# Optimization experiments

Measured on AMD Instinct MI355X. Metric: run time of the kernel, lower is better.

The kernel has to match this reference:

```python
import jax, jax.numpy as jnp
import numpy as np

B, S, D = 64, 512, 768
H, DK, DV = 3, 64, 64
TAG, NBEST = 33, 8
START, STOP = TAG - 2, TAG - 1
NEG = -1e30
LN_EPS = 1e-3


def setup_inputs():
    ks = jax.random.split(jax.random.key(0), 10)
    sc = 0.02
    lengths = jax.random.randint(ks[1], (B,), S // 2, S + 1)
    trans = jax.random.normal(ks[8], (TAG, TAG), jnp.float32) * 0.1
    # NCRF++ constraints: nothing transitions INTO START; nothing OUT of STOP
    trans = trans.at[:, START].set(-10000.0).at[STOP, :].set(-10000.0)
    return {
        "inputs": jax.random.normal(ks[0], (B, S, D), jnp.float32),
        "labels_mask": (jnp.arange(S)[None, :] < lengths[:, None]).astype(jnp.int32),
        "w_qs": jax.random.normal(ks[2], (H, D, DK), jnp.float32) * sc,
        "w_ks": jax.random.normal(ks[3], (H, D, DK), jnp.float32) * sc,
        "w_vs": jax.random.normal(ks[4], (H, D, DV), jnp.float32) * sc,
        "proj_w": jax.random.normal(ks[5], (H * DV, D), jnp.float32) * sc,
        "proj_b": jnp.zeros((D,), jnp.float32),
        "ln_g": jnp.ones((D,), jnp.float32),
        "ln_b": jnp.zeros((D,), jnp.float32),
        "lin1_w": jax.random.normal(ks[6], (D, D // 2), jnp.float32) * sc,
        "lin1_b": jnp.zeros((D // 2,), jnp.float32),
        "lin2_w": jax.random.normal(ks[7], (D // 2, TAG), jnp.float32) * sc,
        "lin2_b": jnp.zeros((TAG,), jnp.float32),
        "transitions": trans,
    }


def _layer_norm(x, g, b):
    mu = jnp.mean(x, -1, keepdims=True)
    sig = jnp.std(x, -1, keepdims=True, ddof=1)  # repo LayerNorm uses unbiased std, eps=1e-3
    return (x - mu) / (sig + LN_EPS) * g + b


def _forward_model(x, w_qs, w_ks, w_vs, proj_w, proj_b, ln_g, ln_b, lin1_w, lin1_b, lin2_w, lin2_b):
    # multi-head attention (mask=None on this path; dropout off: module calls self.eval())
    q = jnp.einsum("bsd,hdk->bhsk", x, w_qs)
    k = jnp.einsum("bsd,hdk->bhsk", x, w_ks)
    v = jnp.einsum("bsd,hdv->bhsv", x, w_vs)
    attn = jax.nn.softmax(jnp.einsum("bhqk,bhtk->bhqt", q, k) / np.float32(np.sqrt(DK)), axis=-1)
    o = jnp.einsum("bhqt,bhtv->bqhv", attn, v).reshape(B, S, H * DV)
    o = _layer_norm(o @ proj_w + proj_b + x, ln_g, ln_b)  # proj + residual + LN
    h = jnp.tanh(o @ lin1_w + lin1_b)                      # Linears hidden (tanh)
    return h @ lin2_w + lin2_b                             # (B, S, TAG)


def _viterbi_dp(logits, mask, transitions):
    # scores[t,b,from,to] = logits[t,b,to] + transitions[from,to]
    scores = logits.transpose(1, 0, 2)[:, :, None, :] + transitions[None, None]  # (S,B,T,T)
    # step-0 partition: only nbest slot 0 is live (NEG elsewhere reproduces torch's idx==1 special case)
    partition0 = jnp.full((B, TAG, NBEST), NEG, logits.dtype).at[:, :, 0].set(scores[0, :, START, :])
    mask_t = mask.astype(jnp.int32).T  # (S, B)

    def step(partition, xs):
        sc_t, m_t = xs  # (B,T,T), (B,)
        cand = (sc_t[:, :, None, :] + partition[:, :, :, None]).reshape(B, TAG * NBEST, TAG)
        vals, idx = jax.lax.top_k(cand.transpose(0, 2, 1), NBEST)  # (B, to, NBEST) over from*nbest
        bp = jnp.where(m_t[:, None, None] > 0, idx, 0)
        return vals, (vals, bp)

    _, (parts, bps) = jax.lax.scan(step, partition0, (scores[1:], mask_t[1:]))
    ph = jnp.concatenate([partition0[None], parts], 0).transpose(1, 0, 2, 3)  # (B,S,T,N)
    last_pos = mask_t.sum(0) - 1  # (B,)
    last_partition = jnp.take_along_axis(ph, last_pos[:, None, None, None], axis=1)[:, 0]  # (B,T,N)
    last_values = (last_partition[:, :, :, None] + transitions[None, :, None, :]).reshape(B, TAG * NBEST, TAG)
    end_vals, end_bp = jax.lax.top_k(last_values.transpose(0, 2, 1), NBEST)  # (B, to, NBEST)
    path_score = jax.nn.softmax(end_vals[:, STOP, :], axis=1)  # (B, NBEST)
    pointer0 = end_bp[:, STOP, :]  # (B, NBEST) index into from*nbest
    return path_score, pointer0, bps, last_pos, mask_t


def _backtrace(pointer0, bps, last_pos, mask_t):
    back_points = jnp.concatenate([bps, jnp.zeros((1, B, TAG, NBEST), bps.dtype)], 0).transpose(1, 0, 2, 3)  # (B,S,T,N)
    ins = jnp.broadcast_to(pointer0[:, None, None, :], (B, S, TAG, NBEST))
    tgrid = jnp.arange(S)[None, :, None, None]
    back_points = jnp.where(tgrid == last_pos[:, None, None, None], ins, back_points)
    bp_flat = back_points.reshape(B, S, TAG * NBEST).transpose(1, 0, 2)  # (S,B,T*N)
    inv = 1 - mask_t  # (S,B), inverted mask used in torch backtrace

    def bt_step(pointer, xs):
        bp_t, inv_t = xs
        new_p = jnp.take_along_axis(bp_t, pointer, axis=1)
        return new_p + pointer * inv_t[:, None], new_p // NBEST

    _, decs = jax.lax.scan(bt_step, pointer0, (bp_flat[:-1], inv[:-1]), reverse=True)
    decode = jnp.concatenate([decs, (pointer0 // NBEST)[None]], 0)  # (S,B,N)
    return decode.transpose(1, 0, 2)  # (B,S,N)


def reference(inputs, labels_mask, w_qs, w_ks, w_vs, proj_w, proj_b, ln_g, ln_b, lin1_w, lin1_b, lin2_w, lin2_b, transitions):
    logits = _forward_model(inputs, w_qs, w_ks, w_vs, proj_w, proj_b, ln_g, ln_b, lin1_w, lin1_b, lin2_w, lin2_b)
    _, pointer0, bps, last_pos, mask_t = _viterbi_dp(logits, labels_mask, transitions)
    decode = _backtrace(pointer0, bps, last_pos, mask_t)
    return decode[:, :, 0]  # preds = best path labels, (B, S)
```

## Files before the change

kernel.cpp:

```cpp
#include <hip/hip_runtime.h>
#include <stdint.h>

typedef float v2f __attribute__((ext_vector_type(2)));

namespace {
constexpr int kB = 64, kS = 512, kD = 768, kH = 3, kDK = 64;
constexpr int kTAG = 33, kNB = 8, kSTART = 31, kSTOP = 32;
constexpr float kNEG = -1e30f;
constexpr size_t kHead = (size_t)kB * kH * kS * kDK;
constexpr size_t kQOFF = 0, kKOFF = kHead, kVOFF = 2 * kHead, kOAOFF = 3 * kHead;
constexpr size_t kWsNeed = 4 * kHead * sizeof(float);
constexpr size_t kBpsByte = (size_t)kB * kS * kTAG * 4;
}

__global__ __launch_bounds__(256) void k_qkv(
    const float* __restrict__ X, const float* __restrict__ wq,
    const float* __restrict__ wk, const float* __restrict__ wv,
    float* __restrict__ ws)
{
  __shared__ __align__(16) float As[32][260];
  __shared__ __align__(16) float Bs[32][68];
  const int bx = blockIdx.y;
  const int m0 = blockIdx.x * 256;
  const int tid = threadIdx.x;
  const int tx = tid & 7, ty = tid >> 3;
  const int typ = bx / 3, h = bx % 3;
  const float* wptr = (typ == 0) ? wq : (typ == 1) ? wk : wv;
  float* outp = ws + ((typ == 0) ? kQOFF : (typ == 1) ? kKOFF : kVOFF);

  v2f acc2[8][4] = {};
  const int r0 = ty * 8, c0 = tx * 8;
  for (int k0 = 0; k0 < kD; k0 += 32) {
    #pragma unroll
    for (int q = 0; q < 8; ++q) {
      const int flat = q * 256 + tid;
      const int r = flat >> 3, kc = (flat & 7) * 4;
      const float4 v = *(const float4*)(X + (size_t)(m0 + r) * kD + k0 + kc);
      As[kc + 0][r] = v.x; As[kc + 1][r] = v.y; As[kc + 2][r] = v.z; As[kc + 3][r] = v.w;
    }
    #pragma unroll
    for (int q = 0; q < 2; ++q) {
      const int flat = q * 256 + tid;
      const int kk = flat >> 4, c4 = (flat & 15) * 4;
      *(float4*)&Bs[kk][c4] =
          *(const float4*)(wptr + ((size_t)h * kD + k0 + kk) * 64 + c4);
    }
    __syncthreads();
    #pragma unroll
    for (int kk = 0; kk < 32; ++kk) {
      const float4 a0 = *(const float4*)&As[kk][r0];
      const float4 a1 = *(const float4*)&As[kk][r0 + 4];
      const float4 b0 = *(const float4*)&Bs[kk][c0];
      const float4 b1 = *(const float4*)&Bs[kk][c0 + 4];
      const float a[8] = {a0.x, a0.y, a0.z, a0.w, a1.x, a1.y, a1.z, a1.w};
      const v2f bp[4] = {{b0.x, b0.y}, {b0.z, b0.w}, {b1.x, b1.y}, {b1.z, b1.w}};
      #pragma unroll
      for (int i = 0; i < 8; ++i) {
        const v2f ai = {a[i], a[i]};
        #pragma unroll
        for (int jj = 0; jj < 4; ++jj)
          acc2[i][jj] = __builtin_elementwise_fma(ai, bp[jj], acc2[i][jj]);
      }
    }
    __syncthreads();
  }
  #pragma unroll
  for (int i = 0; i < 8; ++i) {
    const int m = m0 + r0 + i;
    const int b = m >> 9, s = m & 511;
    float* dst = outp + ((size_t)(b * kH + h) * kS + s) * kDK + c0;
    *(float4*)dst = make_float4(acc2[i][0].x, acc2[i][0].y, acc2[i][1].x, acc2[i][1].y);
    *(float4*)(dst + 4) = make_float4(acc2[i][2].x, acc2[i][2].y, acc2[i][3].x, acc2[i][3].y);
  }
}

__global__ __launch_bounds__(256) void k_attn(
    const float* __restrict__ Q, const float* __restrict__ K,
    const float* __restrict__ V, float* __restrict__ oa)
{
  __shared__ float Qt[64][68];
  __shared__ float Kt[64][68];
  __shared__ float Vl[64][68];
  __shared__ float Pl[64][68];
  const int qt = blockIdx.z, h = blockIdx.y, b = blockIdx.x;
  const int tid = threadIdx.x;
  const int tx = tid & 15, ty = tid >> 4;
  const int r0 = ty * 4, c0 = tx * 4;
  const size_t base = (size_t)(b * kH + h) * kS * kDK;

  {
    const int row = tid >> 2, cc = (tid & 3) * 4;
    const float* src = Q + base + (size_t)(qt * 64 + row) * kDK;
    #pragma unroll
    for (int q = 0; q < 4; ++q) {
      const int c = cc + q * 16;
      const float4 v = *(const float4*)(src + c);
      Qt[c + 0][row] = v.x; Qt[c + 1][row] = v.y; Qt[c + 2][row] = v.z; Qt[c + 3][row] = v.w;
    }
  }
  float m_r[4], l_r[4];
  v2f O2[4][2];
  #pragma unroll
  for (int i = 0; i < 4; ++i) {
    m_r[i] = -__builtin_huge_valf(); l_r[i] = 0.f;
    O2[i][0] = (v2f){0.f, 0.f}; O2[i][1] = (v2f){0.f, 0.f};
  }
  for (int kt = 0; kt < 8; ++kt) {
    __syncthreads();
    {
      const int row = tid >> 2, cc = (tid & 3) * 4;
      const float* srck = K + base + (size_t)(kt * 64 + row) * kDK;
      const float* srcv = V + base + (size_t)(kt * 64 + row) * kDK;
      #pragma unroll
      for (int q = 0; q < 4; ++q) {
        const int c = cc + q * 16;
        const float4 v = *(const float4*)(srck + c);
        Kt[c + 0][row] = v.x; Kt[c + 1][row] = v.y; Kt[c + 2][row] = v.z; Kt[c + 3][row] = v.w;
        *(float4*)&Vl[row][c] = *(const float4*)(srcv + c);
      }
    }
    __syncthreads();
    v2f sc2[4][2] = {};
    for (int k = 0; k < 64; ++k) {
      const float4 a = *(const float4*)&Qt[k][r0];
      const float4 bb = *(const float4*)&Kt[k][c0];
      const float av[4] = {a.x, a.y, a.z, a.w};
      const v2f b01 = {bb.x, bb.y}, b23 = {bb.z, bb.w};
      #pragma unroll
      for (int i = 0; i < 4; ++i) {
        const v2f ai = {av[i], av[i]};
        sc2[i][0] = __builtin_elementwise_fma(ai, b01, sc2[i][0]);
        sc2[i][1] = __builtin_elementwise_fma(ai, b23, sc2[i][1]);
      }
    }
    float sc[4][4];
    #pragma unroll
    for (int i = 0; i < 4; ++i) {
      sc[i][0] = sc2[i][0].x; sc[i][1] = sc2[i][0].y;
      sc[i][2] = sc2[i][1].x; sc[i][3] = sc2[i][1].y;
    }
    #pragma unroll
    for (int i = 0; i < 4; ++i) {
      #pragma unroll
      for (int j = 0; j < 4; ++j) sc[i][j] *= 0.125f;
      float tm = fmaxf(fmaxf(sc[i][0], sc[i][1]), fmaxf(sc[i][2], sc[i][3]));
      #pragma unroll
      for (int m = 1; m < 16; m <<= 1) tm = fmaxf(tm, __shfl_xor(tm, m, 16));
      const float mn = fmaxf(m_r[i], tm);
      const float corr = expf(m_r[i] - mn);
      float ts = 0.f;
      #pragma unroll
      for (int j = 0; j < 4; ++j) { sc[i][j] = expf(sc[i][j] - mn); ts += sc[i][j]; }
      #pragma unroll
      for (int m = 1; m < 16; m <<= 1) ts += __shfl_xor(ts, m, 16);
      l_r[i] = l_r[i] * corr + ts;
      m_r[i] = mn;
      const v2f c2 = {corr, corr};
      O2[i][0] = O2[i][0] * c2;
      O2[i][1] = O2[i][1] * c2;
    }
    #pragma unroll
    for (int j = 0; j < 4; ++j)
      *(float4*)&Pl[c0 + j][r0] = make_float4(sc[0][j], sc[1][j], sc[2][j], sc[3][j]);
    __syncthreads();
    for (int c = 0; c < 64; ++c) {
      const float4 a = *(const float4*)&Pl[c][r0];
      const float4 bb = *(const float4*)&Vl[c][c0];
      const float av[4] = {a.x, a.y, a.z, a.w};
      const v2f b01 = {bb.x, bb.y}, b23 = {bb.z, bb.w};
      #pragma unroll
      for (int i = 0; i < 4; ++i) {
        const v2f ai = {av[i], av[i]};
        O2[i][0] = __builtin_elementwise_fma(ai, b01, O2[i][0]);
        O2[i][1] = __builtin_elementwise_fma(ai, b23, O2[i][1]);
      }
    }
  }
  #pragma unroll
  for (int i = 0; i < 4; ++i) {
    const int s = qt * 64 + r0 + i;
    *(float4*)(oa + ((size_t)(b * kS + s) * kH + h) * 64 + c0) =
        make_float4(O2[i][0].x / l_r[i], O2[i][0].y / l_r[i],
                    O2[i][1].x / l_r[i], O2[i][1].y / l_r[i]);
  }
}

__global__ __launch_bounds__(256) void k_head(
    const float* __restrict__ X, const float* __restrict__ oa,
    const float* __restrict__ pw, const float* __restrict__ pb,
    const float* __restrict__ lng, const float* __restrict__ lnb,
    const float* __restrict__ w1, const float* __restrict__ b1,
    const float* __restrict__ w2, const float* __restrict__ b2,
    float* __restrict__ logits)
{
  constexpr int XLP = 776;
  constexpr int OALP = 200;
  constexpr int HLP = 392;
  __shared__ __align__(16) float xl[16 * XLP];
  __shared__ __align__(16) float uni[16 * HLP];
  const int tid = threadIdx.x;
  const int row0 = blockIdx.x * 16;
  {
    const int r = tid >> 4, seg = tid & 15;
    const float* src = X + (size_t)(row0 + r) * kD;
    #pragma unroll
    for (int q = 0; q < 12; ++q) {
      const int c4 = seg + q * 16;
      *(float4*)&xl[r * XLP + c4 * 4] = *(const float4*)(src + c4 * 4);
    }
    const float* srco = oa + (size_t)(row0 + r) * 192;
    #pragma unroll
    for (int q = 0; q < 3; ++q) {
      const int c4 = seg + q * 16;
      *(float4*)&uni[r * OALP + c4 * 4] = *(const float4*)(srco + c4 * 4);
    }
  }
  __syncthreads();
  if (tid < 192) {
    const int cc = tid * 4;
    v2f accA[16] = {}, accB[16] = {};
    for (int k = 0; k < 192; k += 4) {
      v2f wA[4], wB[4];
      #pragma unroll
      for (int q = 0; q < 4; ++q) {
        wA[q] = *(const v2f*)(pw + (size_t)(k + q) * kD + cc);
        wB[q] = *(const v2f*)(pw + (size_t)(k + q) * kD + cc + 2);
      }
      #pragma unroll
      for (int r = 0; r < 16; ++r) {
        const float4 o4 = *(const float4*)&uni[r * OALP + k];
        accA[r] = __builtin_elementwise_fma((v2f){o4.x, o4.x}, wA[0], accA[r]);
        accB[r] = __builtin_elementwise_fma((v2f){o4.x, o4.x}, wB[0], accB[r]);
        accA[r] = __builtin_elementwise_fma((v2f){o4.y, o4.y}, wA[1], accA[r]);
        accB[r] = __builtin_elementwise_fma((v2f){o4.y, o4.y}, wB[1], accB[r]);
        accA[r] = __builtin_elementwise_fma((v2f){o4.z, o4.z}, wA[2], accA[r]);
        accB[r] = __builtin_elementwise_fma((v2f){o4.z, o4.z}, wB[2], accB[r]);
        accA[r] = __builtin_elementwise_fma((v2f){o4.w, o4.w}, wA[3], accA[r]);
        accB[r] = __builtin_elementwise_fma((v2f){o4.w, o4.w}, wB[3], accB[r]);
      }
    }
    const v2f pbA = *(const v2f*)(pb + cc);
    const v2f pbB = *(const v2f*)(pb + cc + 2);
    #pragma unroll
    for (int r = 0; r < 16; ++r) {
      const float4 res = *(const float4*)&xl[r * XLP + cc];
      const v2f oA = accA[r] + pbA + (v2f){res.x, res.y};
      const v2f oB = accB[r] + pbB + (v2f){res.z, res.w};
      *(float4*)&xl[r * XLP + cc] = make_float4(oA.x, oA.y, oB.x, oB.y);
    }
  }
  __syncthreads();
  {
    const int rr = tid >> 4, g = tid & 15;
    float sm = 0.f;
    #pragma unroll
    for (int q = 0; q < 48; ++q) sm += xl[rr * XLP + g + q * 16];
    #pragma unroll
    for (int m = 1; m < 16; m <<= 1) sm += __shfl_xor(sm, m, 16);
    const float mu = sm / 768.0f;
    float s2 = 0.f;
    #pragma unroll
    for (int q = 0; q < 48; ++q) { const float d = xl[rr * XLP + g + q * 16] - mu; s2 += d * d; }
    #pragma unroll
    for (int m = 1; m < 16; m <<= 1) s2 += __shfl_xor(s2, m, 16);
    const float den = sqrtf(s2 / 767.0f) + 1e-3f;
    #pragma unroll
    for (int q = 0; q < 48; ++q) {
      const int c = g + q * 16;
      xl[rr * XLP + c] = (xl[rr * XLP + c] - mu) / den * lng[c] + lnb[c];
    }
  }
  __syncthreads();
  if (tid < 192) {
    const int cc = tid * 2;
    v2f acc2[16] = {};
    for (int k = 0; k < 768; k += 4) {
      v2f w2[4];
      #pragma unroll
      for (int q = 0; q < 4; ++q)
        w2[q] = *(const v2f*)(w1 + (size_t)(k + q) * 384 + cc);
      #pragma unroll
      for (int r = 0; r < 16; ++r) {
        const float4 x4 = *(const float4*)&xl[r * XLP + k];
        acc2[r] = __builtin_elementwise_fma((v2f){x4.x, x4.x}, w2[0], acc2[r]);
        acc2[r] = __builtin_elementwise_fma((v2f){x4.y, x4.y}, w2[1], acc2[r]);
        acc2[r] = __builtin_elementwise_fma((v2f){x4.z, x4.z}, w2[2], acc2[r]);
        acc2[r] = __builtin_elementwise_fma((v2f){x4.w, x4.w}, w2[3], acc2[r]);
      }
    }
    const v2f bv2 = *(const v2f*)(b1 + cc);
    #pragma unroll
    for (int r = 0; r < 16; ++r) {
      uni[r * HLP + cc + 0] = tanhf(acc2[r].x + bv2.x);
      uni[r * HLP + cc + 1] = tanhf(acc2[r].y + bv2.y);
    }
  }
  __syncthreads();
  for (int idx = tid; idx < 16 * kTAG; idx += 256) {
    const int r = idx / kTAG, j = idx - r * kTAG;
    float acc = 0.f;
    for (int k = 0; k < 384; k += 4) {
      const float4 h4 = *(const float4*)&uni[r * HLP + k];
      acc += h4.x * w2[(size_t)(k + 0) * kTAG + j];
      acc += h4.y * w2[(size_t)(k + 1) * kTAG + j];
      acc += h4.z * w2[(size_t)(k + 2) * kTAG + j];
      acc += h4.w * w2[(size_t)(k + 3) * kTAG + j];
    }
    logits[(size_t)(row0 + r) * kTAG + j] = acc + b2[j];
  }
}

__device__ __forceinline__ double vk_keyd(float v, unsigned idxf) {
  unsigned u = __float_as_uint(v);
  u = (u & 0x80000000u) ? ~u : (u | 0x80000000u);
  const unsigned long long k = ((unsigned long long)u << 31) | idxf;
  return __longlong_as_double((long long)k);
}
__device__ __forceinline__ float vk_vald(double d) {
  const unsigned long long k = (unsigned long long)__double_as_longlong(d);
  unsigned u = (unsigned)(k >> 31);
  u = (u & 0x80000000u) ? (u & 0x7fffffffu) : ~u;
  return __uint_as_float(u);
}
__device__ __forceinline__ int vk_idxd(double d) {
  const unsigned long long k = (unsigned long long)__double_as_longlong(d);
  return (int)(0x7FFFFFFFu - ((unsigned)k & 0x7FFFFFFFu));
}
template <int CTRL>
__device__ __forceinline__ double dppd(double v) {
  const unsigned long long k = (unsigned long long)__double_as_longlong(v);
  const unsigned lo = (unsigned)__builtin_amdgcn_update_dpp((int)(unsigned)k, (int)(unsigned)k, CTRL, 0xF, 0xF, false);
  const unsigned hi = (unsigned)__builtin_amdgcn_update_dpp((int)(unsigned)(k >> 32), (int)(unsigned)(k >> 32), CTRL, 0xF, 0xF, false);
  return __longlong_as_double((long long)(((unsigned long long)hi << 32) | lo));
}
__device__ __forceinline__ void cedd(double& a, double& b) {
  const double mx = fmax(a, b), mn = fmin(a, b);
  a = mx; b = mn;
}
template <int CTRL>
__device__ __forceinline__ void bmerged(double a[8]) {
  double b[8];
  #pragma unroll
  for (int i = 0; i < 8; ++i) b[i] = dppd<CTRL>(a[i]);
  double w[8];
  #pragma unroll
  for (int i = 0; i < 8; ++i) w[i] = fmax(a[i], b[7 - i]);
  cedd(w[0], w[4]); cedd(w[1], w[5]); cedd(w[2], w[6]); cedd(w[3], w[7]);
  cedd(w[0], w[2]); cedd(w[1], w[3]); cedd(w[4], w[6]); cedd(w[5], w[7]);
  cedd(w[0], w[1]); cedd(w[2], w[3]); cedd(w[4], w[5]); cedd(w[6], w[7]);
  #pragma unroll
  for (int i = 0; i < 8; ++i) a[i] = w[i];
}

template <bool WITHLG>
__device__ __forceinline__ void merge31(
    const float (*rows)[12], const float* trans_colj, float lg,
    const float tr[4], const int ii[4], const bool vld[4],
    bool g1, bool g2, bool g4,
    float vout[8], int iout[8])
{
  double a[8];
  #pragma unroll
  for (int c = 0; c < 4; ++c) {
    const float s = WITHLG ? (lg + tr[c]) : tr[c];
    a[c] = vld[c] ? vk_keyd(s + rows[ii[c]][0], 0x7FFFFFFFu - (unsigned)(ii[c] * 8)) : 0.0;
  }
  a[4] = a[5] = a[6] = a[7] = 0.0;
  cedd(a[0], a[2]); cedd(a[1], a[3]); cedd(a[0], a[1]); cedd(a[2], a[3]); cedd(a[1], a[2]);
  bmerged<0xB1>(a);
  bmerged<0x4E>(a);
  bmerged<0x141>(a);
  const unsigned l0 = (unsigned)__double_as_longlong(a[0]);
  const unsigned l1 = (unsigned)__double_as_longlong(a[1]);
  const unsigned l2 = (unsigned)__double_as_longlong(a[2]);
  const unsigned l3 = (unsigned)__double_as_longlong(a[3]);
  const unsigned l4 = (unsigned)__double_as_longlong(a[4]);
  const unsigned l5 = (unsigned)__double_as_longlong(a[5]);
  const unsigned l6 = (unsigned)__double_as_longlong(a[6]);
  const unsigned l7 = (unsigned)__double_as_longlong(a[7]);
  const unsigned lo01 = g1 ? l1 : l0;
  const unsigned lo23 = g1 ? l3 : l2;
  const unsigned lo45 = g1 ? l5 : l4;
  const unsigned lo67 = g1 ? l7 : l6;
  const unsigned loA = g2 ? lo23 : lo01;
  const unsigned loB = g2 ? lo67 : lo45;
  const unsigned sel = (g4 ? loB : loA) & 0x7FFFFFFFu;
  const int L = (int)((0x7FFFFFFFu - sel) >> 3);
  const float trL = trans_colj[(size_t)L * kTAG];
  const float sB = WITHLG ? (lg + trL) : trL;
  const float4* prow = (const float4*)&rows[L][0];
  const float4 r0 = prow[0], r1 = prow[1];
  const unsigned nb = 0x7FFFFFFFu - (unsigned)(L << 3);
  double q[8];
  q[0] = vk_keyd(sB + r0.x, nb - 0); q[1] = vk_keyd(sB + r0.y, nb - 1);
  q[2] = vk_keyd(sB + r0.z, nb - 2); q[3] = vk_keyd(sB + r0.w, nb - 3);
  q[4] = vk_keyd(sB + r1.x, nb - 4); q[5] = vk_keyd(sB + r1.y, nb - 5);
  q[6] = vk_keyd(sB + r1.z, nb - 6); q[7] = vk_keyd(sB + r1.w, nb - 7);
  bmerged<0xB1>(q);
  bmerged<0x4E>(q);
  bmerged<0x141>(q);
  #pragma unroll
  for (int r = 0; r < 8; ++r) {
    vout[r] = vk_vald(q[r]);
    iout[r] = vk_idxd(q[r]);
  }
}

__global__ __launch_bounds__(256) void k_viterbi(
    const float* __restrict__ logits, const int* __restrict__ mask,
    const float* __restrict__ trans, unsigned short* __restrict__ bps,
    int* __restrict__ lastpos_g, int* __restrict__ ptr0_g)
{
  constexpr int kNT = 31;
  __shared__ __align__(16) float trans_s[kTAG][kTAG];
  __shared__ __align__(16) float part[2][kNT][12];
  __shared__ __align__(16) float lastp[kNT][12];
  __shared__ int lastpos_s;
  const int b = blockIdx.x, tid = threadIdx.x;
  for (int idx = tid; idx < kTAG * kTAG; idx += 256)
    trans_s[idx / kTAG][idx % kTAG] = trans[idx];
  if (tid < 64) {
    int sm = 0;
    #pragma unroll
    for (int q = 0; q < 8; ++q) sm += mask[b * kS + tid * 8 + q];
    #pragma unroll
    for (int m = 1; m < 64; m <<= 1) sm += __shfl_xor(sm, m, 64);
    if (tid == 0) { lastpos_s = sm - 1; lastpos_g[b] = sm - 1; }
  }
  const int grp = tid >> 3, g = tid & 7;
  const bool active = (grp < kNT);
  const int j = grp;
  const bool g1 = g & 1, g2 = g & 2, g4 = g & 4;
  __syncthreads();
  float tr[4]; int ii[4]; bool vld[4];
  #pragma unroll
  for (int c = 0; c < 4; ++c) {
    const int i0 = g + 8 * c;
    vld[c] = (i0 < kNT);
    ii[c] = vld[c] ? i0 : 0;
    tr[c] = trans_s[ii[c]][j];
  }
  if (active)
    part[0][j][g] = (g == 0) ? (logits[(size_t)b * kS * kTAG + j] + trans_s[kSTART][j]) : kNEG;
  const int lp = lastpos_s;
  float lg_next = logits[((size_t)b * kS + 1) * kTAG + j];

  for (int t = 1; t < kS; ++t) {
    __syncthreads();
    if (t <= lp) {
      const float lg = lg_next;
      if (t + 1 <= lp) lg_next = logits[((size_t)b * kS + t + 1) * kTAG + j];
      if (active) {
        float vout[8]; int iout[8];
        merge31<true>(part[(t - 1) & 1], &trans_s[0][j], lg, tr, ii, vld, g1, g2, g4, vout, iout);
        if (g == 0) {
          *(float4*)&part[t & 1][j][0] = make_float4(vout[0], vout[1], vout[2], vout[3]);
          *(float4*)&part[t & 1][j][4] = make_float4(vout[4], vout[5], vout[6], vout[7]);
          if (t == lp) {
            *(float4*)&lastp[j][0] = make_float4(vout[0], vout[1], vout[2], vout[3]);
            *(float4*)&lastp[j][4] = make_float4(vout[4], vout[5], vout[6], vout[7]);
          }
          const unsigned w01 = (unsigned)iout[0] | ((unsigned)iout[1] << 16);
          const unsigned w23 = (unsigned)iout[2] | ((unsigned)iout[3] << 16);
          const unsigned w45 = (unsigned)iout[4] | ((unsigned)iout[5] << 16);
          const unsigned w67 = (unsigned)iout[6] | ((unsigned)iout[7] << 16);
          *(int4*)(bps + ((size_t)t * kB + b) * (kTAG * kNB) + j * kNB) =
              make_int4((int)w01, (int)w23, (int)w45, (int)w67);
        }
      }
    } else if (active && g == 0) {
      *(int4*)(bps + ((size_t)t * kB + b) * (kTAG * kNB) + j * kNB) = make_int4(0, 0, 0, 0);
    }
  }
  __syncthreads();
  if (tid < 8) {
    float tre[4];
    #pragma unroll
    for (int c = 0; c < 4; ++c) tre[c] = trans_s[ii[c]][kSTOP];
    float vo[8]; int io[8];
    merge31<false>(lastp, &trans_s[0][kSTOP], 0.f, tre, ii, vld, g1, g2, g4, vo, io);
    if (tid == 0) {
      *(int4*)&ptr0_g[b * kNB + 0] = make_int4(io[0], io[1], io[2], io[3]);
      *(int4*)&ptr0_g[b * kNB + 4] = make_int4(io[4], io[5], io[6], io[7]);
    }
  }
}

__global__ __launch_bounds__(256) void k_backtrace(
    const unsigned short* __restrict__ bps, const int* __restrict__ ptr0,
    const int* __restrict__ lastpos, const int* __restrict__ mask,
    int* __restrict__ out)
{
  __shared__ uint4 buf[2][4][33];
  __shared__ int ptr0_s[kNB];
  __shared__ int mask_s[kS];
  const int b = blockIdx.x, tid = threadIdx.x;
  if (tid < kNB) ptr0_s[tid] = ptr0[b * kNB + tid];
  for (int i = tid; i < kS; i += 256) mask_s[i] = mask[b * kS + i];
  const int lp = lastpos[b];
  const int lr = tid / 33, lc = tid % 33;
  if (tid < 132)
    buf[0][lr][lc] = ((const uint4*)(bps + ((size_t)(kS - 1 - lr) * kB + b) * (kTAG * kNB)))[lc];
  int p = ptr0[b * kNB];
  if (tid == 0) out[b * kS + kS - 1] = p >> 3;
  __syncthreads();
  int cur = 0, tau = kS - 2;
  while (tau >= 0) {
    const int cnt = (tau >= 3) ? 4 : (tau + 1);
    const int ntau = tau - cnt;
    uint4 v; bool have = false;
    if (ntau >= 0 && tid < 132) {
      const int cnt2 = (ntau >= 3) ? 4 : (ntau + 1);
      if (lr < cnt2) {
        v = ((const uint4*)(bps + ((size_t)(ntau + 1 - lr) * kB + b) * (kTAG * kNB)))[lc];
        have = true;
      }
    }
    for (int s2 = 0; s2 < cnt; ++s2) {
      const int t2 = tau - s2;
      int np;
      if (t2 == lp) np = ptr0_s[p & 7];
      else np = ((const unsigned short*)&buf[cur][s2][0])[p];
      if (tid == 0) out[b * kS + t2] = np >> 3;
      p = mask_s[t2] ? np : (np + p);
    }
    __syncthreads();
    if (have) buf[cur ^ 1][lr][lc] = v;
    __syncthreads();
    cur ^= 1; tau = ntau;
  }
}

extern "C" void kernel_launch(void* const* d_in, const int* in_sizes, int n_in,
                              void* d_out, int out_size, void* d_ws, size_t ws_size,
                              hipStream_t stream) {
  if (ws_size < kWsNeed) return;
  const float* X   = (const float*)d_in[0];
  const int*   msk = (const int*)d_in[1];
  const float* wq  = (const float*)d_in[2];
  const float* wk  = (const float*)d_in[3];
  const float* wv  = (const float*)d_in[4];
  const float* pw  = (const float*)d_in[5];
  const float* pb  = (const float*)d_in[6];
  const float* lng = (const float*)d_in[7];
  const float* lnb = (const float*)d_in[8];
  const float* w1  = (const float*)d_in[9];
  const float* b1  = (const float*)d_in[10];
  const float* w2  = (const float*)d_in[11];
  const float* b2  = (const float*)d_in[12];
  const float* trn = (const float*)d_in[13];
  float* ws = (float*)d_ws;

  k_qkv<<<dim3(128, 9), 256, 0, stream>>>(X, wq, wk, wv, ws);
  k_attn<<<dim3(64, 3, 8), 256, 0, stream>>>(ws + kQOFF, ws + kKOFF, ws + kVOFF, ws + kOAOFF);
  k_head<<<2048, 256, 0, stream>>>(X, ws + kOAOFF, pw, pb, lng, lnb, w1, b1, w2, b2, ws);
  unsigned short* bps = (unsigned short*)((char*)d_ws + kBpsByte);
  int* lastpos_p = (int*)(ws + kKOFF);
  int* ptr0_p = lastpos_p + kB;
  k_viterbi<<<kB, 256, 0, stream>>>(ws, msk, trn, bps, lastpos_p, ptr0_p);
  k_backtrace<<<kB, 256, 0, stream>>>(bps, ptr0_p, lastpos_p, msk, (int*)d_out);
}
```

Measured before the change: 1.993 ms.

## Software-pipeline Viterbi step by computing next step's head-argmax ahead

Splits the per-step top-k merge into two phases. Phase A picks the best predecessor from the row heads. Phase B merges that predecessor's 8-best row. Phase A for step t+1 now runs during step t, using a separate shared heads array, so the serial chain inside each barrier-separated step gets shorter. The cost is an extra shared array, more register pressure, and a more complex loop-carried state.

```diff
diff --git a/kernel.cpp b/kernel.cpp
--- a/kernel.cpp
+++ b/kernel.cpp
@@ -350,6 +350,61 @@
   cedd(w[0], w[1]); cedd(w[2], w[3]); cedd(w[4], w[5]); cedd(w[6], w[7]);
   #pragma unroll
   for (int i = 0; i < 8; ++i) a[i] = w[i];
+}
+
+__device__ __forceinline__ int phaseA_d(
+    const float* __restrict__ heads, float lg,
+    const float tr[4], const int ii[4], const bool vld[4],
+    bool g1, bool g2, bool g4, float* newhead)
+{
+  double a[8];
+  #pragma unroll
+  for (int c = 0; c < 4; ++c) {
+    const float s = lg + tr[c];
+    a[c] = vld[c] ? vk_keyd(s + heads[ii[c]], 0x7FFFFFFFu - (unsigned)(ii[c] * 8)) : 0.0;
+  }
+  a[4] = a[5] = a[6] = a[7] = 0.0;
+  cedd(a[0], a[2]); cedd(a[1], a[3]); cedd(a[0], a[1]); cedd(a[2], a[3]); cedd(a[1], a[2]);
+  bmerged<0xB1>(a);
+  bmerged<0x4E>(a);
+  bmerged<0x141>(a);
+  *newhead = vk_vald(a[0]);
+  const unsigned l0 = (unsigned)__double_as_longlong(a[0]);
+  const unsigned l1 = (unsigned)__double_as_longlong(a[1]);
+  const unsigned l2 = (unsigned)__double_as_longlong(a[2]);
+  const unsigned l3 = (unsigned)__double_as_longlong(a[3]);
+  const unsigned l4 = (unsigned)__double_as_longlong(a[4]);
+  const unsigned l5 = (unsigned)__double_as_longlong(a[5]);
+  const unsigned l6 = (unsigned)__double_as_longlong(a[6]);
+  const unsigned l7 = (unsigned)__double_as_longlong(a[7]);
+  const unsigned lo01 = g1 ? l1 : l0;
+  const unsigned lo23 = g1 ? l3 : l2;
+  const unsigned lo45 = g1 ? l5 : l4;
+  const unsigned lo67 = g1 ? l7 : l6;
+  const unsigned loA = g2 ? lo23 : lo01;
+  const unsigned loB = g2 ? lo67 : lo45;
+  const unsigned sel = (g4 ? loB : loA) & 0x7FFFFFFFu;
+  return (int)((0x7FFFFFFFu - sel) >> 3);
+}
+
+__device__ __forceinline__ void phaseB_d(
+    float4 r0, float4 r1, float sB, int L,
+    float vout[8], int iout[8])
+{
+  const unsigned nb = 0x7FFFFFFFu - (unsigned)(L << 3);
+  double q[8];
+  q[0] = vk_keyd(sB + r0.x, nb - 0); q[1] = vk_keyd(sB + r0.y, nb - 1);
+  q[2] = vk_keyd(sB + r0.z, nb - 2); q[3] = vk_keyd(sB + r0.w, nb - 3);
+  q[4] = vk_keyd(sB + r1.x, nb - 4); q[5] = vk_keyd(sB + r1.y, nb - 5);
+  q[6] = vk_keyd(sB + r1.z, nb - 6); q[7] = vk_keyd(sB + r1.w, nb - 7);
+  bmerged<0xB1>(q);
+  bmerged<0x4E>(q);
+  bmerged<0x141>(q);
+  #pragma unroll
+  for (int r = 0; r < 8; ++r) {
+    vout[r] = vk_vald(q[r]);
+    iout[r] = vk_idxd(q[r]);
+  }
 }
 
 template <bool WITHLG>
@@ -389,21 +444,7 @@
   const float trL = trans_colj[(size_t)L * kTAG];
   const float sB = WITHLG ? (lg + trL) : trL;
   const float4* prow = (const float4*)&rows[L][0];
-  const float4 r0 = prow[0], r1 = prow[1];
-  const unsigned nb = 0x7FFFFFFFu - (unsigned)(L << 3);
-  double q[8];
-  q[0] = vk_keyd(sB + r0.x, nb - 0); q[1] = vk_keyd(sB + r0.y, nb - 1);
-  q[2] = vk_keyd(sB + r0.z, nb - 2); q[3] = vk_keyd(sB + r0.w, nb - 3);
-  q[4] = vk_keyd(sB + r1.x, nb - 4); q[5] = vk_keyd(sB + r1.y, nb - 5);
-  q[6] = vk_keyd(sB + r1.z, nb - 6); q[7] = vk_keyd(sB + r1.w, nb - 7);
-  bmerged<0xB1>(q);
-  bmerged<0x4E>(q);
-  bmerged<0x141>(q);
-  #pragma unroll
-  for (int r = 0; r < 8; ++r) {
-    vout[r] = vk_vald(q[r]);
-    iout[r] = vk_idxd(q[r]);
-  }
+  phaseB_d(prow[0], prow[1], sB, L, vout, iout);
 }
 
 __global__ __launch_bounds__(256) void k_viterbi(
@@ -415,6 +456,7 @@
   __shared__ __align__(16) float trans_s[kTAG][kTAG];
   __shared__ __align__(16) float part[2][kNT][12];
   __shared__ __align__(16) float lastp[kNT][12];
+  __shared__ float heads_s[2][kNT + 1];
   __shared__ int lastpos_s;
   const int b = blockIdx.x, tid = threadIdx.x;
   for (int idx = tid; idx < kTAG * kTAG; idx += 256)
@@ -440,19 +482,41 @@
     ii[c] = vld[c] ? i0 : 0;
     tr[c] = trans_s[ii[c]][j];
   }
-  if (active)
-    part[0][j][g] = (g == 0) ? (logits[(size_t)b * kS * kTAG + j] + trans_s[kSTART][j]) : kNEG;
+  if (active) {
+    const float h0 = logits[(size_t)b * kS * kTAG + j] + trans_s[kSTART][j];
+    part[0][j][g] = (g == 0) ? h0 : kNEG;
+    if (g == 0) heads_s[0][j] = h0;
+  }
   const int lp = lastpos_s;
-  float lg_next = logits[((size_t)b * kS + 1) * kTAG + j];
+  __syncthreads();
+
+  int L_cur = 0;
+  float lgB = 0.f, lgA = 0.f;
+  if (active) {
+    const float lg1 = logits[((size_t)b * kS + 1) * kTAG + j];
+    float nh;
+    L_cur = phaseA_d(heads_s[0], lg1, tr, ii, vld, g1, g2, g4, &nh);
+    if (g == 0) heads_s[1][j] = nh;
+    lgB = lg1;
+    lgA = logits[((size_t)b * kS + 2) * kTAG + j];
+  }
 
   for (int t = 1; t < kS; ++t) {
     __syncthreads();
     if (t <= lp) {
-      const float lg = lg_next;
-      if (t + 1 <= lp) lg_next = logits[((size_t)b * kS + t + 1) * kTAG + j];
       if (active) {
+        const float4* prow = (const float4*)&part[(t - 1) & 1][L_cur][0];
+        const float4 rA = prow[0], rB = prow[1];
+        const float trL = trans_s[L_cur][j];
+        int L_next = L_cur;
+        if (t + 1 <= lp) {
+          float nh;
+          L_next = phaseA_d(heads_s[t & 1], lgA, tr, ii, vld, g1, g2, g4, &nh);
+          if (g == 0) heads_s[(t + 1) & 1][j] = nh;
+        }
+        const float lgP = (t + 2 < kS) ? logits[((size_t)b * kS + t + 2) * kTAG + j] : 0.f;
         float vout[8]; int iout[8];
-        merge31<true>(part[(t - 1) & 1], &trans_s[0][j], lg, tr, ii, vld, g1, g2, g4, vout, iout);
+        phaseB_d(rA, rB, lgB + trL, L_cur, vout, iout);
         if (g == 0) {
           *(float4*)&part[t & 1][j][0] = make_float4(vout[0], vout[1], vout[2], vout[3]);
           *(float4*)&part[t & 1][j][4] = make_float4(vout[4], vout[5], vout[6], vout[7]);
@@ -467,6 +531,7 @@
           *(int4*)(bps + ((size_t)t * kB + b) * (kTAG * kNB) + j * kNB) =
               make_int4((int)w01, (int)w23, (int)w45, (int)w67);
         }
+        L_cur = L_next; lgB = lgA; lgA = lgP;
       }
     } else if (active && g == 0) {
       *(int4*)(bps + ((size_t)t * kB + b) * (kTAG * kNB) + j * kNB) = make_int4(0, 0, 0, 0);
```

Result: no change. 1.999 ms (+0.3%).
